# Optimization experiments

Hardware: AMD Instinct MI355X
Metric: run time of the kernel (lower is better)

## Reference

```python
import jax, jax.numpy as jnp
import numpy as np

V = 786432        # 12 * nside^2, nside=256
E = 8 * V         # ~8-neighbor HEALPix graph Laplacian nnz
KSIZE = 5         # Chebyshev polynomial order
FIN = 16
FOUT = 32
B = 1


def _spmm(rows, cols, vals, z):
    # sparse [V,V] @ dense [V,F] via gather + segment-sum
    return jax.ops.segment_sum(vals[:, None] * z[cols], rows, num_segments=V)


def _cheb_conv(rows, cols, vals, x, weight, bias):
    # x: [B, V, Fin]; weight: [Fin*K, Fout]
    b, v, fin = x.shape
    x0 = jnp.transpose(x, (1, 2, 0)).reshape(v, fin * b)  # [V, Fin*B]
    xs = [x0]
    if KSIZE > 1:
        x1 = _spmm(rows, cols, vals, x0)
        xs.append(x1)
        for _ in range(2, KSIZE):
            x2 = 2.0 * _spmm(rows, cols, vals, x1) - x0
            xs.append(x2)
            x0, x1 = x1, x2
    stack = jnp.stack(xs)                                  # [K, V, Fin*B]
    stack = stack.reshape(KSIZE, v, fin, b)
    stack = jnp.transpose(stack, (3, 1, 2, 0)).reshape(b * v, fin * KSIZE)
    out = stack @ weight + bias                            # [B*V, Fout]
    return out.reshape(b, v, -1)


def setup_inputs() -> dict:
    key = jax.random.key(0)
    ks = jax.random.split(key, 8)
    x = jax.random.normal(ks[0], (B, V, FIN), dtype=jnp.float32)
    lap_rows = jax.random.randint(ks[1], (E,), 0, V, dtype=jnp.int32)
    lap_cols = jax.random.randint(ks[2], (E,), 0, V, dtype=jnp.int32)
    lap_vals = jax.random.normal(ks[3], (E,), dtype=jnp.float32) * 0.1
    w1 = jax.random.normal(ks[4], (FIN * KSIZE, FOUT), dtype=jnp.float32) * (1.0 / np.sqrt(FIN * KSIZE))
    b1 = jax.random.normal(ks[5], (FOUT,), dtype=jnp.float32) * 0.01
    w2 = jax.random.normal(ks[6], (FOUT * KSIZE, FOUT), dtype=jnp.float32) * (1.0 / np.sqrt(FOUT * KSIZE))
    b2 = jax.random.normal(ks[7], (FOUT,), dtype=jnp.float32) * 0.01
    return {"x": x, "lap_rows": lap_rows, "lap_cols": lap_cols, "lap_vals": lap_vals,
            "w1": w1, "b1": b1, "w2": w2, "b2": b2}


def reference(x, lap_rows, lap_cols, lap_vals, w1, b1, w2, b2):
    h = _cheb_conv(lap_rows, lap_cols, lap_vals, x, w1, b1)
    h = jax.nn.elu(h, alpha=1.0)
    h = _cheb_conv(lap_rows, lap_cols, lap_vals, h, w2, b2)
    skip = jax.nn.elu(h, alpha=1.0)                         # [B, V, Fout]
    # HealpixMaxPool: nested ordering -> factor-4 pooling along vertex dim
    pooled = skip.reshape(B, V // 4, 4, FOUT).max(axis=2)   # [B, V/4, Fout]
    return (skip, pooled)
```

## Files before the change

kernel.cpp:

```cpp
#include <hip/hip_runtime.h>
#include <hip/hip_bf16.h>

#define VN 786432
#define EN 6291456
#define KCH 5
#define FIN 16
#define FOUT 32


__global__ void k_count(const int4* __restrict__ rows4, int* __restrict__ cnt) {
    int i = blockIdx.x * blockDim.x + threadIdx.x;
    int4 r = rows4[i];
    atomicAdd(&cnt[r.x], 1);
    atomicAdd(&cnt[r.y], 1);
    atomicAdd(&cnt[r.z], 1);
    atomicAdd(&cnt[r.w], 1);
}

__global__ void k_scan(const int* __restrict__ cnt, int* __restrict__ row_start,
                       int* __restrict__ cursor, int* __restrict__ gcur) {
    int i = blockIdx.x * blockDim.x + threadIdx.x;
    int lane = threadIdx.x & 63;
    int c = cnt[i];
    int s = c;
    #pragma unroll
    for (int d = 1; d < 64; d <<= 1) {
        int t = __shfl_up(s, d);
        if (lane >= d) s += t;
    }
    int total = __shfl(s, 63);
    int base = 0;
    if (lane == 63) base = atomicAdd(gcur, total);
    base = __shfl(base, 63);
    int st = base + s - c;
    row_start[i] = st;
    cursor[i] = st;
}

__global__ void k_fill(const int4* __restrict__ rows4, const int4* __restrict__ cols4,
                       const float4* __restrict__ vals4, int* __restrict__ cursor,
                       int2* __restrict__ csr) {
    int i = blockIdx.x * blockDim.x + threadIdx.x;
    int4 r = rows4[i]; int4 c = cols4[i]; float4 v = vals4[i];
    int p;
    p = atomicAdd(&cursor[r.x], 1); csr[p] = make_int2(c.x, __float_as_int(v.x));
    p = atomicAdd(&cursor[r.y], 1); csr[p] = make_int2(c.y, __float_as_int(v.y));
    p = atomicAdd(&cursor[r.z], 1); csr[p] = make_int2(c.z, __float_as_int(v.z));
    p = atomicAdd(&cursor[r.w], 1); csr[p] = make_int2(c.w, __float_as_int(v.w));
}


template<int F, bool FIRST, bool LAST, bool POOL>
__global__ void k_spmm_fused(const int* __restrict__ row_start, const int* __restrict__ cnt,
                             const int2* __restrict__ csr,
                             const float* __restrict__ z, const float* __restrict__ prev,
                             const float* __restrict__ w, const float* __restrict__ bias,
                             float* __restrict__ h, float* __restrict__ xout,
                             float* __restrict__ pooled, int k) {
    constexpr int C = F / 4;
    constexpr int HPL = FOUT / C;
    __shared__ float lds[POOL ? (256 / (F / 4)) * FOUT : 1];

    int t = blockIdx.x * blockDim.x + threadIdx.x;
    int row = t / C, ch = t % C;
    int lane = threadIdx.x & 63;
    int gbase = lane & ~(C - 1);

    int s = row_start[row], n = cnt[row];
    float4 acc = make_float4(0.f, 0.f, 0.f, 0.f);
    for (int j = 0; j < n; ++j) {
        int2 e = csr[s + j];
        float v = __int_as_float(e.y);
        const float4 zz = *reinterpret_cast<const float4*>(&z[(size_t)e.x * F + ch * 4]);
        acc.x += v * zz.x; acc.y += v * zz.y; acc.z += v * zz.z; acc.w += v * zz.w;
    }
    const float4 pr = *reinterpret_cast<const float4*>(&prev[(size_t)row * F + ch * 4]);
    float4 xk;
    if (FIRST) {
        xk = acc;
    } else {
        xk = make_float4(2.f * acc.x - pr.x, 2.f * acc.y - pr.y,
                         2.f * acc.z - pr.z, 2.f * acc.w - pr.w);
    }
    if (!LAST) *reinterpret_cast<float4*>(&xout[(size_t)row * F + ch * 4]) = xk;

    float xr[F];
    float x0r[FIRST ? F : 1];
    #pragma unroll
    for (int c2 = 0; c2 < C; ++c2) {
        int src = gbase + c2;
        xr[c2 * 4 + 0] = __shfl(xk.x, src);
        xr[c2 * 4 + 1] = __shfl(xk.y, src);
        xr[c2 * 4 + 2] = __shfl(xk.z, src);
        xr[c2 * 4 + 3] = __shfl(xk.w, src);
        if (FIRST) {
            x0r[c2 * 4 + 0] = __shfl(pr.x, src);
            x0r[c2 * 4 + 1] = __shfl(pr.y, src);
            x0r[c2 * 4 + 2] = __shfl(pr.z, src);
            x0r[c2 * 4 + 3] = __shfl(pr.w, src);
        }
    }

    int fo0 = ch * HPL;
    float hacc[HPL];
    if (FIRST) {
        #pragma unroll
        for (int i = 0; i < HPL; ++i) hacc[i] = bias[fo0 + i];
    } else {
        #pragma unroll
        for (int i = 0; i < HPL; i += 4) {
            float4 hv = *reinterpret_cast<const float4*>(&h[(size_t)row * FOUT + fo0 + i]);
            hacc[i] = hv.x; hacc[i + 1] = hv.y; hacc[i + 2] = hv.z; hacc[i + 3] = hv.w;
        }
    }
    #pragma unroll
    for (int f = 0; f < F; ++f) {
        const float* wrow = &w[(f * KCH + k) * FOUT + fo0];
        #pragma unroll
        for (int i = 0; i < HPL; ++i) hacc[i] += xr[f] * wrow[i];
    }
    if (FIRST) {
        #pragma unroll
        for (int f = 0; f < F; ++f) {
            const float* wrow = &w[(f * KCH + 0) * FOUT + fo0];
            #pragma unroll
            for (int i = 0; i < HPL; ++i) hacc[i] += x0r[f] * wrow[i];
        }
    }
    if (LAST) {
        #pragma unroll
        for (int i = 0; i < HPL; ++i)
            hacc[i] = hacc[i] > 0.f ? hacc[i] : (expf(hacc[i]) - 1.f);
    }
    #pragma unroll
    for (int i = 0; i < HPL; i += 4) {
        *reinterpret_cast<float4*>(&h[(size_t)row * FOUT + fo0 + i]) =
            make_float4(hacc[i], hacc[i + 1], hacc[i + 2], hacc[i + 3]);
    }
    if (POOL) {
        int rl = threadIdx.x / C;
        #pragma unroll
        for (int i = 0; i < HPL; ++i) lds[rl * FOUT + fo0 + i] = hacc[i];
        __syncthreads();
        int pvl = threadIdx.x >> 5;
        int f = threadIdx.x & 31;
        float m = lds[(pvl * 4 + 0) * FOUT + f];
        m = fmaxf(m, lds[(pvl * 4 + 1) * FOUT + f]);
        m = fmaxf(m, lds[(pvl * 4 + 2) * FOUT + f]);
        m = fmaxf(m, lds[(pvl * 4 + 3) * FOUT + f]);
        pooled[(size_t)(blockIdx.x * 8 + pvl) * FOUT + f] = m;
    }
}

extern "C" void kernel_launch(void* const* d_in, const int* in_sizes, int n_in,
                              void* d_out, int out_size, void* d_ws, size_t ws_size,
                              hipStream_t stream) {
    const float* x    = (const float*)d_in[0];
    const int*   rows = (const int*)  d_in[1];
    const int*   cols = (const int*)  d_in[2];
    const float* vals = (const float*)d_in[3];
    const float* w1   = (const float*)d_in[4];
    const float* b1   = (const float*)d_in[5];
    const float* w2   = (const float*)d_in[6];
    const float* b2   = (const float*)d_in[7];
    float* out = (float*)d_out;

    float* bufA      = (float*)d_ws;
    float* bufB      = bufA + (size_t)VN * FOUT;
    float* h1        = bufB + (size_t)VN * FOUT;
    int2*  csr       = (int2*)(h1 + (size_t)VN * FOUT);
    int*   row_start = (int*)(csr + EN);
    int*   cnt       = row_start + VN;
    int*   cursor    = cnt + VN;
    int*   gcur      = cursor + VN;

    hipMemsetAsync(cnt, 0, VN * sizeof(int), stream);
    hipMemsetAsync(gcur, 0, sizeof(int), stream);

    const int B = 256;
    k_count<<<EN / 4 / B, B, 0, stream>>>((const int4*)rows, cnt);
    k_scan <<<VN / B, B, 0, stream>>>(cnt, row_start, cursor, gcur);
    k_fill <<<EN / 4 / B, B, 0, stream>>>((const int4*)rows, (const int4*)cols,
                                          (const float4*)vals, cursor, csr);

    const int g16 = VN * (FIN / 4) / B;
    const int g32 = VN * (FOUT / 4) / B;

    k_spmm_fused<FIN, true,  false, false><<<g16, B, 0, stream>>>(
        row_start, cnt, csr, x,    x,    w1, b1, h1, bufA, nullptr, 1);
    k_spmm_fused<FIN, false, false, false><<<g16, B, 0, stream>>>(
        row_start, cnt, csr, bufA, x,    w1, b1, h1, bufB, nullptr, 2);
    k_spmm_fused<FIN, false, false, false><<<g16, B, 0, stream>>>(
        row_start, cnt, csr, bufB, bufA, w1, b1, h1, bufA, nullptr, 3);
    k_spmm_fused<FIN, false, true,  false><<<g16, B, 0, stream>>>(
        row_start, cnt, csr, bufA, bufB, w1, b1, h1, nullptr, nullptr, 4);

    k_spmm_fused<FOUT, true,  false, false><<<g32, B, 0, stream>>>(
        row_start, cnt, csr, h1,   h1,   w2, b2, out, bufA, nullptr, 1);
    k_spmm_fused<FOUT, false, false, false><<<g32, B, 0, stream>>>(
        row_start, cnt, csr, bufA, h1,   w2, b2, out, bufB, nullptr, 2);
    k_spmm_fused<FOUT, false, false, false><<<g32, B, 0, stream>>>(
        row_start, cnt, csr, bufB, bufA, w2, b2, out, bufA, nullptr, 3);
    k_spmm_fused<FOUT, false, true,  true ><<<g32, B, 0, stream>>>(
        row_start, cnt, csr, bufA, bufB, w2, b2, out, nullptr,
        out + (size_t)VN * FOUT, 4);
}
```

Measured before the change: 2.707 ms.

## Store Chebyshev intermediates and gather operands in bf16 with 8-wide lanes

Converts the input features and all Chebyshev intermediate buffers (and the layer-1 activation) to packed bf16, so each sparse gather reads half the bytes. Each thread now handles 8 features via a uint4 load instead of 4 floats, which halves the number of threads per row and changes the pooling index mapping. Accumulation and the weight projection stay in fp32. In exchange it adds an extra conversion kernel and rounding error in the intermediates that may exceed tolerance. Workspace is repacked with aliased regions to fit the new buffers.

```diff
diff --git a/kernel.cpp b/kernel.cpp
--- a/kernel.cpp
+++ b/kernel.cpp
@@ -7,6 +7,15 @@
 #define FIN 16
 #define FOUT 32
 
+__device__ inline float blo(unsigned u) { return __uint_as_float(u << 16); }
+__device__ inline float bhi(unsigned u) { return __uint_as_float(u & 0xffff0000u); }
+__device__ inline unsigned bpack(float lo, float hi) {
+    unsigned ul = __float_as_uint(lo), uh = __float_as_uint(hi);
+    ul = (ul + 0x7fffu + ((ul >> 16) & 1u)) >> 16;
+    uh = (uh + 0x7fffu + ((uh >> 16) & 1u)) & 0xffff0000u;
+    return ul | uh;
+}
+
 
 __global__ void k_count(const int4* __restrict__ rows4, int* __restrict__ cnt) {
     int i = blockIdx.x * blockDim.x + threadIdx.x;
@@ -21,7 +30,7 @@
                        int* __restrict__ cursor, int* __restrict__ gcur) {
     int i = blockIdx.x * blockDim.x + threadIdx.x;
     int lane = threadIdx.x & 63;
-    int c = cnt[i];
+    int c = (i < VN) ? cnt[i] : 0;
     int s = c;
     #pragma unroll
     for (int d = 1; d < 64; d <<= 1) {
@@ -33,8 +42,7 @@
     if (lane == 63) base = atomicAdd(gcur, total);
     base = __shfl(base, 63);
     int st = base + s - c;
-    row_start[i] = st;
-    cursor[i] = st;
+    if (i < VN) { row_start[i] = st; cursor[i] = st; }
 }
 
 __global__ void k_fill(const int4* __restrict__ rows4, const int4* __restrict__ cols4,
@@ -49,55 +57,67 @@
     p = atomicAdd(&cursor[r.w], 1); csr[p] = make_int2(c.w, __float_as_int(v.w));
 }
 
-
-template<int F, bool FIRST, bool LAST, bool POOL>
-__global__ void k_spmm_fused(const int* __restrict__ row_start, const int* __restrict__ cnt,
-                             const int2* __restrict__ csr,
-                             const float* __restrict__ z, const float* __restrict__ prev,
-                             const float* __restrict__ w, const float* __restrict__ bias,
-                             float* __restrict__ h, float* __restrict__ xout,
-                             float* __restrict__ pooled, int k) {
-    constexpr int C = F / 4;
+__global__ void k_cvt(const float4* __restrict__ xf, uint4* __restrict__ xb) {
+    int i = blockIdx.x * blockDim.x + threadIdx.x;
+    float4 a = xf[2 * i], b = xf[2 * i + 1];
+    uint4 o;
+    o.x = bpack(a.x, a.y); o.y = bpack(a.z, a.w);
+    o.z = bpack(b.x, b.y); o.w = bpack(b.z, b.w);
+    xb[i] = o;
+}
+
+
+template<int F, bool FIRST, bool LAST, bool HOUT_BF, bool POOL>
+__global__ void k_spmm(const int* __restrict__ row_start, const int* __restrict__ cnt,
+                       const int2* __restrict__ csr,
+                       const uint4* zb, const uint4* prevb,
+                       const float* __restrict__ w, const float* __restrict__ bias,
+                       float* h, uint4* xoutb,
+                       uint4* h1b, float* pooled, int k) {
+    constexpr int C = F / 8;
+    constexpr int LC = (C == 2) ? 1 : 2;
     constexpr int HPL = FOUT / C;
-    __shared__ float lds[POOL ? (256 / (F / 4)) * FOUT : 1];
+    __shared__ float lds[POOL ? (256 / C) * FOUT : 1];
 
     int t = blockIdx.x * blockDim.x + threadIdx.x;
-    int row = t / C, ch = t % C;
+    int row = t >> LC, ch = t & (C - 1);
     int lane = threadIdx.x & 63;
     int gbase = lane & ~(C - 1);
 
     int s = row_start[row], n = cnt[row];
-    float4 acc = make_float4(0.f, 0.f, 0.f, 0.f);
+    float acc[8];
+    #pragma unroll
+    for (int q = 0; q < 8; ++q) acc[q] = 0.f;
     for (int j = 0; j < n; ++j) {
         int2 e = csr[s + j];
         float v = __int_as_float(e.y);
-        const float4 zz = *reinterpret_cast<const float4*>(&z[(size_t)e.x * F + ch * 4]);
-        acc.x += v * zz.x; acc.y += v * zz.y; acc.z += v * zz.z; acc.w += v * zz.w;
-    }
-    const float4 pr = *reinterpret_cast<const float4*>(&prev[(size_t)row * F + ch * 4]);
-    float4 xk;
-    if (FIRST) {
-        xk = acc;
-    } else {
-        xk = make_float4(2.f * acc.x - pr.x, 2.f * acc.y - pr.y,
-                         2.f * acc.z - pr.z, 2.f * acc.w - pr.w);
-    }
-    if (!LAST) *reinterpret_cast<float4*>(&xout[(size_t)row * F + ch * 4]) = xk;
+        uint4 zz = zb[(size_t)e.x * C + ch];
+        acc[0] += v * blo(zz.x); acc[1] += v * bhi(zz.x);
+        acc[2] += v * blo(zz.y); acc[3] += v * bhi(zz.y);
+        acc[4] += v * blo(zz.z); acc[5] += v * bhi(zz.z);
+        acc[6] += v * blo(zz.w); acc[7] += v * bhi(zz.w);
+    }
+    uint4 pv = prevb[(size_t)row * C + ch];
+    float pr[8] = { blo(pv.x), bhi(pv.x), blo(pv.y), bhi(pv.y),
+                    blo(pv.z), bhi(pv.z), blo(pv.w), bhi(pv.w) };
+    float xk[8];
+    #pragma unroll
+    for (int q = 0; q < 8; ++q) xk[q] = FIRST ? acc[q] : 2.f * acc[q] - pr[q];
+    if (!LAST) {
+        uint4 o;
+        o.x = bpack(xk[0], xk[1]); o.y = bpack(xk[2], xk[3]);
+        o.z = bpack(xk[4], xk[5]); o.w = bpack(xk[6], xk[7]);
+        xoutb[(size_t)row * C + ch] = o;
+    }
 
     float xr[F];
     float x0r[FIRST ? F : 1];
     #pragma unroll
     for (int c2 = 0; c2 < C; ++c2) {
-        int src = gbase + c2;
-        xr[c2 * 4 + 0] = __shfl(xk.x, src);
-        xr[c2 * 4 + 1] = __shfl(xk.y, src);
-        xr[c2 * 4 + 2] = __shfl(xk.z, src);
-        xr[c2 * 4 + 3] = __shfl(xk.w, src);
-        if (FIRST) {
-            x0r[c2 * 4 + 0] = __shfl(pr.x, src);
-            x0r[c2 * 4 + 1] = __shfl(pr.y, src);
-            x0r[c2 * 4 + 2] = __shfl(pr.z, src);
-            x0r[c2 * 4 + 3] = __shfl(pr.w, src);
+        #pragma unroll
+        for (int q = 0; q < 8; ++q) {
+            xr[c2 * 8 + q] = __shfl(xk[q], gbase + c2);
+            if (FIRST) x0r[c2 * 8 + q] = __shfl(pr[q], gbase + c2);
         }
     }
 
@@ -132,23 +152,37 @@
         for (int i = 0; i < HPL; ++i)
             hacc[i] = hacc[i] > 0.f ? hacc[i] : (expf(hacc[i]) - 1.f);
     }
-    #pragma unroll
-    for (int i = 0; i < HPL; i += 4) {
-        *reinterpret_cast<float4*>(&h[(size_t)row * FOUT + fo0 + i]) =
-            make_float4(hacc[i], hacc[i + 1], hacc[i + 2], hacc[i + 3]);
+    if (LAST && HOUT_BF) {
+        uint4 o0, o1;
+        o0.x = bpack(hacc[0], hacc[1]);  o0.y = bpack(hacc[2], hacc[3]);
+        o0.z = bpack(hacc[4], hacc[5]);  o0.w = bpack(hacc[6], hacc[7]);
+        o1.x = bpack(hacc[8], hacc[9]);  o1.y = bpack(hacc[10], hacc[11]);
+        o1.z = bpack(hacc[12], hacc[13]); o1.w = bpack(hacc[14], hacc[15]);
+        h1b[(size_t)row * (FOUT / 8) + ch * 2 + 0] = o0;
+        h1b[(size_t)row * (FOUT / 8) + ch * 2 + 1] = o1;
+    } else {
+        #pragma unroll
+        for (int i = 0; i < HPL; i += 4) {
+            *reinterpret_cast<float4*>(&h[(size_t)row * FOUT + fo0 + i]) =
+                make_float4(hacc[i], hacc[i + 1], hacc[i + 2], hacc[i + 3]);
+        }
     }
     if (POOL) {
-        int rl = threadIdx.x / C;
+        int rl = threadIdx.x >> LC;
         #pragma unroll
         for (int i = 0; i < HPL; ++i) lds[rl * FOUT + fo0 + i] = hacc[i];
         __syncthreads();
-        int pvl = threadIdx.x >> 5;
-        int f = threadIdx.x & 31;
-        float m = lds[(pvl * 4 + 0) * FOUT + f];
-        m = fmaxf(m, lds[(pvl * 4 + 1) * FOUT + f]);
-        m = fmaxf(m, lds[(pvl * 4 + 2) * FOUT + f]);
-        m = fmaxf(m, lds[(pvl * 4 + 3) * FOUT + f]);
-        pooled[(size_t)(blockIdx.x * 8 + pvl) * FOUT + f] = m;
+        int pvl = threadIdx.x >> 4;
+        int f0 = (threadIdx.x & 15) * 2;
+        #pragma unroll
+        for (int u = 0; u < 2; ++u) {
+            int f = f0 + u;
+            float m = lds[(pvl * 4 + 0) * FOUT + f];
+            m = fmaxf(m, lds[(pvl * 4 + 1) * FOUT + f]);
+            m = fmaxf(m, lds[(pvl * 4 + 2) * FOUT + f]);
+            m = fmaxf(m, lds[(pvl * 4 + 3) * FOUT + f]);
+            pooled[(size_t)(blockIdx.x * 16 + pvl) * FOUT + f] = m;
+        }
     }
 }
 
@@ -165,14 +199,22 @@
     const float* b2   = (const float*)d_in[7];
     float* out = (float*)d_out;
 
-    float* bufA      = (float*)d_ws;
-    float* bufB      = bufA + (size_t)VN * FOUT;
-    float* h1        = bufB + (size_t)VN * FOUT;
-    int2*  csr       = (int2*)(h1 + (size_t)VN * FOUT);
-    int*   row_start = (int*)(csr + EN);
-    int*   cnt       = row_start + VN;
-    int*   cursor    = cnt + VN;
-    int*   gcur      = cursor + VN;
+    char* p = (char*)d_ws;
+    int2*  csr = (int2*)p;  p += (size_t)EN * 8;
+    uint4* xb  = (uint4*)p; p += (size_t)VN * FIN * 2;
+    char* R = p;            p += (size_t)176160768;
+    float* h1f = (float*)R;
+    uint4* t0  = (uint4*)(R + 100663296);
+    uint4* t1  = (uint4*)(R + 125829120);
+    uint4* t2  = (uint4*)(R + 150994944);
+    uint4* u0  = (uint4*)R;
+    uint4* u1  = (uint4*)(R + 50331648);
+    uint4* u2  = (uint4*)(R + 100663296);
+    uint4* h1b = (uint4*)p; p += (size_t)VN * FOUT * 2;
+    int* row_start = (int*)p; p += (size_t)VN * 4;
+    int* cnt       = (int*)p; p += (size_t)VN * 4;
+    int* cursor    = (int*)p; p += (size_t)VN * 4;
+    int* gcur      = (int*)p;
 
     hipMemsetAsync(cnt, 0, VN * sizeof(int), stream);
     hipMemsetAsync(gcur, 0, sizeof(int), stream);
@@ -183,25 +225,27 @@
     k_fill <<<EN / 4 / B, B, 0, stream>>>((const int4*)rows, (const int4*)cols,
                                           (const float4*)vals, cursor, csr);
 
-    const int g16 = VN * (FIN / 4) / B;
-    const int g32 = VN * (FOUT / 4) / B;
-
-    k_spmm_fused<FIN, true,  false, false><<<g16, B, 0, stream>>>(
-        row_start, cnt, csr, x,    x,    w1, b1, h1, bufA, nullptr, 1);
-    k_spmm_fused<FIN, false, false, false><<<g16, B, 0, stream>>>(
-        row_start, cnt, csr, bufA, x,    w1, b1, h1, bufB, nullptr, 2);
-    k_spmm_fused<FIN, false, false, false><<<g16, B, 0, stream>>>(
-        row_start, cnt, csr, bufB, bufA, w1, b1, h1, bufA, nullptr, 3);
-    k_spmm_fused<FIN, false, true,  false><<<g16, B, 0, stream>>>(
-        row_start, cnt, csr, bufA, bufB, w1, b1, h1, nullptr, nullptr, 4);
-
-    k_spmm_fused<FOUT, true,  false, false><<<g32, B, 0, stream>>>(
-        row_start, cnt, csr, h1,   h1,   w2, b2, out, bufA, nullptr, 1);
-    k_spmm_fused<FOUT, false, false, false><<<g32, B, 0, stream>>>(
-        row_start, cnt, csr, bufA, h1,   w2, b2, out, bufB, nullptr, 2);
-    k_spmm_fused<FOUT, false, false, false><<<g32, B, 0, stream>>>(
-        row_start, cnt, csr, bufB, bufA, w2, b2, out, bufA, nullptr, 3);
-    k_spmm_fused<FOUT, false, true,  true ><<<g32, B, 0, stream>>>(
-        row_start, cnt, csr, bufA, bufB, w2, b2, out, nullptr,
+    k_cvt<<<VN * FIN / 8 / B, B, 0, stream>>>((const float4*)x, xb);
+
+    const int g16 = VN * 2 / B;
+    const int g32 = VN * 4 / B;
+
+    k_spmm<FIN, true,  false, false, false><<<g16, B, 0, stream>>>(
+        row_start, cnt, csr, xb, xb, w1, b1, h1f, t0, nullptr, nullptr, 1);
+    k_spmm<FIN, false, false, false, false><<<g16, B, 0, stream>>>(
+        row_start, cnt, csr, t0, xb, w1, b1, h1f, t1, nullptr, nullptr, 2);
+    k_spmm<FIN, false, false, false, false><<<g16, B, 0, stream>>>(
+        row_start, cnt, csr, t1, t0, w1, b1, h1f, t2, nullptr, nullptr, 3);
+    k_spmm<FIN, false, true,  true,  false><<<g16, B, 0, stream>>>(
+        row_start, cnt, csr, t2, t1, w1, b1, h1f, nullptr, h1b, nullptr, 4);
+
+    k_spmm<FOUT, true,  false, false, false><<<g32, B, 0, stream>>>(
+        row_start, cnt, csr, h1b, h1b, w2, b2, out, u0, nullptr, nullptr, 1);
+    k_spmm<FOUT, false, false, false, false><<<g32, B, 0, stream>>>(
+        row_start, cnt, csr, u0, h1b, w2, b2, out, u1, nullptr, nullptr, 2);
+    k_spmm<FOUT, false, false, false, false><<<g32, B, 0, stream>>>(
+        row_start, cnt, csr, u1, u0, w2, b2, out, u2, nullptr, nullptr, 3);
+    k_spmm<FOUT, false, true,  false, true ><<<g32, B, 0, stream>>>(
+        row_start, cnt, csr, u2, u1, w2, b2, out, nullptr, nullptr,
         out + (size_t)VN * FOUT, 4);
 }
```

Result: faster. 2.639 ms (-2.5%).
